# Kernel tuning notes

Measured on AMD Instinct MI355X. Metric: run time of the kernel, lower is better.

Reference implementation:

```python
import jax, jax.numpy as jnp
import numpy as np

N0, N1, N2 = 512, 2048, 8192   # targets, hop1, hop2 node counts
K = 33                          # nneighbor + self loop
IN, HID, OUT, NH = 256, 128, 128, 8
NEG = -9.0e15
ALPHA = 0.2                     # LeakyReLU negative slope


def setup_inputs() -> dict:
    key = jax.random.key(0)
    ks = jax.random.split(key, 8)
    feats = jax.random.normal(ks[0], (N2, IN), jnp.float32)
    # xavier-ish scaled params (gain 1.414)
    W1 = jax.random.normal(ks[1], (NH, IN, HID), jnp.float32) * 0.072
    a1 = jax.random.normal(ks[2], (NH, 2 * HID), jnp.float32) * 0.105
    W2 = jax.random.normal(ks[3], (HID * NH, OUT), jnp.float32) * 0.042
    a2 = jax.random.normal(ks[4], (2 * OUT,), jnp.float32) * 0.105
    # layer1 edges: each of N1 targets gets K distinct neighbors in [0, N2)
    tgt1 = jnp.repeat(jnp.arange(N1, dtype=jnp.int32), K)
    dst1 = ((jnp.arange(N1)[:, None] * 97 + jnp.arange(K)[None, :] * 131) % N2).astype(jnp.int32).reshape(-1)
    src1 = jax.random.randint(ks[5], (N1 * K,), 0, N2, jnp.int32)
    # layer2 edges: each of N0 targets gets K distinct neighbors in [0, N1)
    tgt2 = jnp.repeat(jnp.arange(N0, dtype=jnp.int32), K)
    dst2 = ((jnp.arange(N0)[:, None] * 53 + jnp.arange(K)[None, :] * 61) % N1).astype(jnp.int32).reshape(-1)
    src2 = jax.random.randint(ks[6], (N0 * K,), 0, N1, jnp.int32)
    return dict(feats=feats, W1=W1, a1=a1, W2=W2, a2=a2,
                src1=src1, dst1=dst1, tgt1=tgt1, src2=src2, dst2=dst2, tgt2=tgt2)


def gat_layer(x, W, a, src, dst, tgt, t_len):
    # x: [n, in], W: [in, d], a: [2d]
    h = x @ W                                   # [n, d]
    d = h.shape[1]
    # concat([h[src], h[dst]]) @ a  ==  h[src]@a[:d] + h[dst]@a[d:]
    e = h[src] @ a[:d] + h[dst] @ a[d:]         # [E]
    e = jnp.where(e > 0, e, ALPHA * e)          # LeakyReLU
    att = jnp.full((t_len, h.shape[0]), NEG, h.dtype).at[tgt, dst].set(e)
    att = jax.nn.softmax(att, axis=1)           # dense row softmax (masked entries ~0)
    return jax.nn.elu(att @ h)                  # [t_len, d]


def reference(feats, W1, a1, W2, a2, src1, dst1, tgt1, src2, dst2, tgt2):
    # layer 1: nhead independent GAT heads over hop2 features
    heads = jax.vmap(lambda W, a: gat_layer(feats, W, a, src1, dst1, tgt1, N1))(W1, a1)  # [NH, N1, HID]
    x = jnp.transpose(heads, (1, 0, 2)).reshape(N1, NH * HID)  # torch.cat(dim=1)
    # layer 2: single GAT layer producing [N0, OUT]
    return gat_layer(x, W2, a2, src2, dst2, tgt2, N0)
```

## Files before the change

### kernel.cpp

```cpp
#include <hip/hip_runtime.h>
#include <math.h>

#define ALPHA 0.2f

constexpr int CN0 = 512, CN1 = 2048, CN2 = 8192, CK = 33;
constexpr int CIN = 256, CHID = 128, CNH = 8;

using u16    = unsigned short;
using f32x4  = __attribute__((ext_vector_type(4))) float;
using bf16x8 = __attribute__((ext_vector_type(8))) short;

__device__ __forceinline__ u16 f2bf(float f) {
    unsigned u = __float_as_uint(f);
    u += 0x7fff + ((u >> 16) & 1);
    return (u16)(u >> 16);
}
__device__ __forceinline__ float bf2f(u16 h) {
    return __uint_as_float(((unsigned)h) << 16);
}

#define GLD16(g, l)                                                        \
    __builtin_amdgcn_global_load_lds(                                      \
        (const __attribute__((address_space(1))) void*)(g),                \
        (__attribute__((address_space(3))) void*)(l), 16, 0, 0)

__global__ __launch_bounds__(256) void prep2_k(const float* __restrict__ W1,
                                               u16* __restrict__ w1t,
                                               const float* __restrict__ W2,
                                               u16* __restrict__ w2t,
                                               const float* __restrict__ a1,
                                               float* __restrict__ pvec) {
    __shared__ float t[32][33];
    int b = blockIdx.x;
    if (b >= 384) {
        const int i = b - 384;
        const int h = i >> 1, half = i & 1;
        const int j = threadIdx.x;
        const float* wrow = W1 + (size_t)h * CIN * CHID + (size_t)j * CHID;
        const float* ah   = a1 + h * 2 * CHID + half * CHID;
        float d = 0.f;
#pragma unroll 8
        for (int c = 0; c < CHID; ++c) d = fmaf(wrow[c], ah[c], d);
        pvec[(h * 2 + half) * CIN + j] = d;
        return;
    }
    const float* ip;
    u16* op;
    int R, C, r0, c0;
    if (b < 256) {
        const int h = b >> 5, w = b & 31;
        ip = W1 + (size_t)h * CIN * CHID;
        op = w1t + (size_t)h * CIN * CHID;
        R = CIN; C = CHID; r0 = (w >> 2) * 32; c0 = (w & 3) * 32;
    } else {
        b -= 256;
        ip = W2; op = w2t;
        R = CNH * CHID; C = CHID; r0 = (b >> 2) * 32; c0 = (b & 3) * 32;
    }
    const int tx = threadIdx.x & 31, ty = threadIdx.x >> 5;
#pragma unroll
    for (int i = 0; i < 4; ++i)
        t[ty + 8 * i][tx] = ip[(size_t)(r0 + ty + 8 * i) * C + c0 + tx];
    __syncthreads();
#pragma unroll
    for (int i = 0; i < 4; ++i)
        op[(size_t)(c0 + ty + 8 * i) * R + r0 + tx] = f2bf(t[tx][ty + 8 * i]);
}

__global__ __launch_bounds__(256) void fsc_k(const float* __restrict__ feats,
                                             u16* __restrict__ fb,
                                             const float* __restrict__ pvec,
                                             float* __restrict__ s1,
                                             float* __restrict__ s2) {
    const int node = (blockIdx.x * 256 + threadIdx.x) >> 6;
    const int lane = threadIdx.x & 63;
    const float4 v = *reinterpret_cast<const float4*>(feats + (size_t)node * CIN + lane * 4);
    *reinterpret_cast<ushort4*>(fb + (size_t)node * CIN + lane * 4) =
        make_ushort4(f2bf(v.x), f2bf(v.y), f2bf(v.z), f2bf(v.w));
#pragma unroll
    for (int h = 0; h < CNH; ++h) {
        const float4 p1 = *reinterpret_cast<const float4*>(pvec + (h * 2 + 0) * CIN + lane * 4);
        const float4 p2 = *reinterpret_cast<const float4*>(pvec + (h * 2 + 1) * CIN + lane * 4);
        float d1 = v.x * p1.x + v.y * p1.y + v.z * p1.z + v.w * p1.w;
        float d2 = v.x * p2.x + v.y * p2.y + v.z * p2.z + v.w * p2.w;
#pragma unroll
        for (int m = 1; m < 64; m <<= 1) {
            d1 += __shfl_xor(d1, m);
            d2 += __shfl_xor(d2, m);
        }
        if (lane == 0) {
            s1[h * CN2 + node] = d1;
            s2[h * CN2 + node] = d2;
        }
    }
}

__global__ __launch_bounds__(128) void agg1g_k(const float* __restrict__ s1,
                                               const float* __restrict__ s2,
                                               const int* __restrict__ src,
                                               const int* __restrict__ dst,
                                               const u16* __restrict__ fb,
                                               u16* __restrict__ gb) {
    __shared__ float wgt[CNH][CK];
    __shared__ int dsts[CK];

    const int t    = blockIdx.x;
    const int tid  = threadIdx.x;
    const int wv   = tid >> 6;
    const int lane = tid & 63;

    int sv = 0, dv = 0;
    if (lane < CK) {
        sv = src[t * CK + lane];
        dv = dst[t * CK + lane];
        if (tid < CK) dsts[tid] = dv;
    }
#pragma unroll
    for (int hh = 0; hh < 4; ++hh) {
        const int head = wv * 4 + hh;
        float e = -3.0e38f;
        if (lane < CK) {
            const float ee = s1[head * CN2 + sv] + s2[head * CN2 + dv];
            e = (ee > 0.f) ? ee : ALPHA * ee;
        }
        float m = e;
#pragma unroll
        for (int mm = 1; mm < 64; mm <<= 1) m = fmaxf(m, __shfl_xor(m, mm));
        const float p = (lane < CK) ? __expf(e - m) : 0.f;
        float s = p;
#pragma unroll
        for (int mm = 1; mm < 64; mm <<= 1) s += __shfl_xor(s, mm);
        if (lane < CK) wgt[head][lane] = p / s;
    }
    __syncthreads();

    const int c2 = tid * 2;
    float acc[CNH][2];
#pragma unroll
    for (int h = 0; h < CNH; ++h) { acc[h][0] = 0.f; acc[h][1] = 0.f; }
#pragma unroll 4
    for (int k = 0; k < CK; ++k) {
        const unsigned w2 = *reinterpret_cast<const unsigned*>(
            fb + (size_t)dsts[k] * CIN + c2);
        const float f0 = bf2f((u16)(w2 & 0xffff));
        const float f1 = bf2f((u16)(w2 >> 16));
#pragma unroll
        for (int h = 0; h < CNH; ++h) {
            const float wk = wgt[h][k];
            acc[h][0] = fmaf(wk, f0, acc[h][0]);
            acc[h][1] = fmaf(wk, f1, acc[h][1]);
        }
    }
#pragma unroll
    for (int h = 0; h < CNH; ++h) {
        const unsigned o = ((unsigned)f2bf(acc[h][1]) << 16) | f2bf(acc[h][0]);
        *reinterpret_cast<unsigned*>(gb + ((size_t)h * CN1 + t) * CIN + c2) = o;
    }
}

__global__ __launch_bounds__(256) void fusedproj_k(const u16* __restrict__ gb,
                                                   const u16* __restrict__ w1t,
                                                   const u16* __restrict__ w2t,
                                                   float* __restrict__ part) {
    __shared__ __attribute__((aligned(16))) char smem[24576];

    const int tid  = threadIdx.x;
    const int lane = tid & 63;
    const int wave = tid >> 6;
    const int trow0 = blockIdx.x * 64;
    const int h     = blockIdx.y;
    const int wr = (wave >> 1) * 32;
    const int wc = (wave & 1) * 64;

    const u16* A  = gb  + (size_t)h * CN1 * CIN;
    const u16* Bt = w1t + (size_t)h * CHID * CIN;

    f32x4 acc[2][4];
#pragma unroll
    for (int m = 0; m < 2; ++m)
#pragma unroll
        for (int n = 0; n < 4; ++n) acc[m][n] = (f32x4){0.f, 0.f, 0.f, 0.f};

    const int r0c = tid >> 2;
    const int cs0 = tid & 3;
    const int c0  = (cs0 - (r0c >> 1)) & 3;
    const int r1c = r0c + 64;

    const u16* ga0 = A + (size_t)(trow0 + r0c) * CIN + c0 * 8;
    const u16* gb0 = Bt + (size_t)r0c * CIN + c0 * 8;
    const u16* gb1 = Bt + (size_t)r1c * CIN + c0 * 8;

    auto STAGE = [&](int s) {
        const int k0 = s * 32;
        char* base = smem + (s & 1) * 12288;
        u16* as = (u16*)base + wave * 512;
        u16* bs = (u16*)(base + 4096) + wave * 512;
        GLD16(ga0 + k0, as);
        GLD16(gb0 + k0, bs);
        GLD16(gb1 + k0, bs + 2048);
    };

    STAGE(0);
    __syncthreads();

    for (int s = 0; s < 8; ++s) {
        if (s + 1 < 8) STAGE(s + 1);

        const u16* Acur = (const u16*)(smem + (s & 1) * 12288);
        const u16* Bcur = Acur + 2048;

        bf16x8 af[2], bfr[4];
#pragma unroll
        for (int m = 0; m < 2; ++m) {
            const int rt = wr + m * 16 + (lane & 15);
            const int cs = ((lane >> 4) + (rt >> 1)) & 3;
            af[m] = *reinterpret_cast<const bf16x8*>(Acur + rt * 32 + cs * 8);
        }
#pragma unroll
        for (int n = 0; n < 4; ++n) {
            const int rt2 = wc + n * 16 + (lane & 15);
            const int cs2 = ((lane >> 4) + (rt2 >> 1)) & 3;
            bfr[n] = *reinterpret_cast<const bf16x8*>(Bcur + rt2 * 32 + cs2 * 8);
        }
#pragma unroll
        for (int m = 0; m < 2; ++m)
#pragma unroll
            for (int n = 0; n < 4; ++n)
                acc[m][n] = __builtin_amdgcn_mfma_f32_16x16x32_bf16(
                    af[m], bfr[n], acc[m][n], 0, 0, 0);

        __syncthreads();
    }

    u16* Xs = (u16*)smem;
#pragma unroll
    for (int m = 0; m < 2; ++m) {
        const int rr = wr + m * 16 + (lane >> 4) * 4;
#pragma unroll
        for (int n = 0; n < 4; ++n) {
            const int cc = wc + n * 16 + (lane & 15);
#pragma unroll
            for (int q = 0; q < 4; ++q) {
                float v = acc[m][n][q];
                v = (v > 0.f) ? v : __expf(v) - 1.f;
                const int r = rr + q;
                Xs[r * 128 + ((((cc >> 3) ^ (r & 7)) << 3) | (cc & 7))] = f2bf(v);
            }
        }
    }
    __syncthreads();

    f32x4 acc2[2][4];
#pragma unroll
    for (int m = 0; m < 2; ++m)
#pragma unroll
        for (int n = 0; n < 4; ++n) acc2[m][n] = (f32x4){0.f, 0.f, 0.f, 0.f};

#pragma unroll
    for (int ks = 0; ks < 4; ++ks) {
        bf16x8 a2f[2], b2f[4];
#pragma unroll
        for (int m = 0; m < 2; ++m) {
            const int rt = wr + m * 16 + (lane & 15);
            const int k0 = ks * 32 + (lane >> 4) * 8;
            a2f[m] = *reinterpret_cast<const bf16x8*>(
                Xs + rt * 128 + (((k0 >> 3) ^ (rt & 7)) << 3));
        }
#pragma unroll
        for (int n = 0; n < 4; ++n) {
            const int rb = wc + n * 16 + (lane & 15);
            b2f[n] = *reinterpret_cast<const bf16x8*>(
                w2t + (size_t)rb * (CNH * CHID) + h * CHID + ks * 32 + (lane >> 4) * 8);
        }
#pragma unroll
        for (int m = 0; m < 2; ++m)
#pragma unroll
            for (int n = 0; n < 4; ++n)
                acc2[m][n] = __builtin_amdgcn_mfma_f32_16x16x32_bf16(
                    a2f[m], b2f[n], acc2[m][n], 0, 0, 0);
    }

#pragma unroll
    for (int m = 0; m < 2; ++m) {
        const int rr = trow0 + wr + m * 16 + (lane >> 4) * 4;
#pragma unroll
        for (int n = 0; n < 4; ++n) {
            const int cc = wc + n * 16 + (lane & 15);
#pragma unroll
            for (int q = 0; q < 4; ++q)
                part[((size_t)h * CN1 + rr + q) * CHID + cc] = acc2[m][n][q];
        }
    }
}

__global__ __launch_bounds__(256) void scores2_k(const float* __restrict__ part,
                                                 const float* __restrict__ a,
                                                 float* __restrict__ h2,
                                                 float* __restrict__ s1,
                                                 float* __restrict__ s2) {
    const int wid  = (blockIdx.x * 256 + threadIdx.x) >> 6;
    const int lane = threadIdx.x & 63;
    const int j = lane * 2;
    float x0 = 0.f, x1 = 0.f;
#pragma unroll
    for (int sp = 0; sp < 8; ++sp) {
        const float2 v = *reinterpret_cast<const float2*>(
            part + (size_t)sp * CN1 * CHID + (size_t)wid * CHID + j);
        x0 += v.x; x1 += v.y;
    }
    *reinterpret_cast<float2*>(h2 + (size_t)wid * CHID + j) = make_float2(x0, x1);
    float d1 = x0 * a[j] + x1 * a[j + 1];
    float d2 = x0 * a[CHID + j] + x1 * a[CHID + j + 1];
#pragma unroll
    for (int m = 1; m < 64; m <<= 1) {
        d1 += __shfl_xor(d1, m);
        d2 += __shfl_xor(d2, m);
    }
    if (lane == 0) { s1[wid] = d1; s2[wid] = d2; }
}

__global__ __launch_bounds__(256) void agg2_k(const float* __restrict__ s1,
                                              const float* __restrict__ s2,
                                              const int* __restrict__ src,
                                              const int* __restrict__ dst,
                                              const float* __restrict__ h2,
                                              float* __restrict__ out) {
    const int t    = (blockIdx.x * 256 + threadIdx.x) >> 6;
    const int lane = threadIdx.x & 63;

    float e = -3.0e38f;
    int dv = 0;
    if (lane < CK) {
        const int sv = src[t * CK + lane];
        dv = dst[t * CK + lane];
        const float ee = s1[sv] + s2[dv];
        e = (ee > 0.f) ? ee : ALPHA * ee;
    }
    float m = e;
#pragma unroll
    for (int mm = 1; mm < 64; mm <<= 1) m = fmaxf(m, __shfl_xor(m, mm));
    float p = (lane < CK) ? __expf(e - m) : 0.f;
    float ssum = p;
#pragma unroll
    for (int mm = 1; mm < 64; mm <<= 1) ssum += __shfl_xor(ssum, mm);
    const float invs = 1.f / ssum;

    float a0 = 0.f, a1 = 0.f;
#pragma unroll
    for (int k = 0; k < CK; ++k) {
        const float w = __shfl(p, k) * invs;
        const int d = __shfl(dv, k);
        const float2 hv = *reinterpret_cast<const float2*>(h2 + (size_t)d * CHID + lane * 2);
        a0 = fmaf(w, hv.x, a0);
        a1 = fmaf(w, hv.y, a1);
    }
    a0 = (a0 > 0.f) ? a0 : __expf(a0) - 1.f;
    a1 = (a1 > 0.f) ? a1 : __expf(a1) - 1.f;
    *reinterpret_cast<float2*>(out + (size_t)t * CHID + lane * 2) = make_float2(a0, a1);
}

extern "C" void kernel_launch(void* const* d_in, const int* in_sizes, int n_in,
                              void* d_out, int out_size, void* d_ws, size_t ws_size,
                              hipStream_t stream) {
    const float* feats = (const float*)d_in[0];
    const float* W1    = (const float*)d_in[1];
    const float* a1    = (const float*)d_in[2];
    const float* W2    = (const float*)d_in[3];
    const float* a2    = (const float*)d_in[4];
    const int*   src1  = (const int*)d_in[5];
    const int*   dst1  = (const int*)d_in[6];
    const int*   src2  = (const int*)d_in[8];
    const int*   dst2  = (const int*)d_in[9];
    float* out = (float*)d_out;

    char* w = (char*)d_ws;
    u16*   fb   = (u16*)w;                 w += (size_t)CN2 * CIN * 2;
    u16*   w1t  = (u16*)w;                 w += (size_t)CNH * CIN * CHID * 2;
    u16*   w2t  = (u16*)w;                 w += (size_t)CNH * CHID * CHID * 2;
    float* pvec = (float*)w;               w += (size_t)CNH * 2 * CIN * 4;
    float* s1   = (float*)w;               w += (size_t)CNH * CN2 * 4;
    float* s2   = (float*)w;               w += (size_t)CNH * CN2 * 4;
    u16*   gb   = (u16*)w;                 w += (size_t)CNH * CN1 * CIN * 2;
    float* part = (float*)w;               w += (size_t)8 * CN1 * CHID * 4;
    float* h2   = (float*)w;               w += (size_t)CN1 * CHID * 4;
    float* s21  = (float*)w;               w += (size_t)CN1 * 4;
    float* s22  = (float*)w;               w += (size_t)CN1 * 4;

    prep2_k<<<dim3(256 + 128 + 16), 256, 0, stream>>>(W1, w1t, W2, w2t, a1, pvec);

    fsc_k<<<dim3(CN2 / 4), 256, 0, stream>>>(feats, fb, pvec, s1, s2);

    agg1g_k<<<dim3(CN1), 128, 0, stream>>>(s1, s2, src1, dst1, fb, gb);

    fusedproj_k<<<dim3(CN1 / 64, CNH), 256, 0, stream>>>(gb, w1t, w2t, part);

    scores2_k<<<dim3(CN1 / 4), 256, 0, stream>>>(part, a2, h2, s21, s22);

    agg2_k<<<dim3(CN0 / 4), 256, 0, stream>>>(s21, s22, src2, dst2, h2, out);
}
```

Baseline: 52.81 us.

## Fuse head loop into projection kernel, accumulate layer-2 in registers, fold scores

The projection kernel now loops over all 8 heads inside one block of 32 rows and accumulates the second-layer product in registers. This removes the per-head partial buffer and the separate reduction/score kernel, which now runs as an epilogue computing h2 and the attention score dot products. The weight transpose is also merged into the feature-conversion kernel, and pvec gets its own small kernel. In exchange the projection grid drops from 256 blocks to 64, which lowers parallelism and lengthens the serial K loop per block.

```diff
diff --git a/kernel.cpp b/kernel.cpp
--- a/kernel.cpp
+++ b/kernel.cpp
@@ -24,26 +24,55 @@
         (const __attribute__((address_space(1))) void*)(g),                \
         (__attribute__((address_space(3))) void*)(l), 16, 0, 0)
 
-__global__ __launch_bounds__(256) void prep2_k(const float* __restrict__ W1,
-                                               u16* __restrict__ w1t,
-                                               const float* __restrict__ W2,
-                                               u16* __restrict__ w2t,
-                                               const float* __restrict__ a1,
-                                               float* __restrict__ pvec) {
+__global__ __launch_bounds__(256) void pvec_k(const float* __restrict__ W1,
+                                              const float* __restrict__ a1,
+                                              float* __restrict__ pvec) {
+    const int h = blockIdx.x >> 1, half = blockIdx.x & 1;
+    const int j = threadIdx.x;
+    const float* wrow = W1 + (size_t)h * CIN * CHID + (size_t)j * CHID;
+    const float* ah   = a1 + h * 2 * CHID + half * CHID;
+    float d = 0.f;
+#pragma unroll 8
+    for (int c = 0; c < CHID; ++c) d = fmaf(wrow[c], ah[c], d);
+    pvec[(h * 2 + half) * CIN + j] = d;
+}
+
+__global__ __launch_bounds__(256) void fsc_k(const float* __restrict__ feats,
+                                             u16* __restrict__ fb,
+                                             const float* __restrict__ pvec,
+                                             float* __restrict__ s1,
+                                             float* __restrict__ s2,
+                                             const float* __restrict__ W1,
+                                             u16* __restrict__ w1t,
+                                             const float* __restrict__ W2,
+                                             u16* __restrict__ w2t) {
     __shared__ float t[32][33];
     int b = blockIdx.x;
-    if (b >= 384) {
-        const int i = b - 384;
-        const int h = i >> 1, half = i & 1;
-        const int j = threadIdx.x;
-        const float* wrow = W1 + (size_t)h * CIN * CHID + (size_t)j * CHID;
-        const float* ah   = a1 + h * 2 * CHID + half * CHID;
-        float d = 0.f;
-#pragma unroll 8
-        for (int c = 0; c < CHID; ++c) d = fmaf(wrow[c], ah[c], d);
-        pvec[(h * 2 + half) * CIN + j] = d;
+    if (b < 2048) {
+        const int node = (b * 256 + threadIdx.x) >> 6;
+        const int lane = threadIdx.x & 63;
+        const float4 v = *reinterpret_cast<const float4*>(feats + (size_t)node * CIN + lane * 4);
+        *reinterpret_cast<ushort4*>(fb + (size_t)node * CIN + lane * 4) =
+            make_ushort4(f2bf(v.x), f2bf(v.y), f2bf(v.z), f2bf(v.w));
+#pragma unroll
+        for (int h = 0; h < CNH; ++h) {
+            const float4 p1 = *reinterpret_cast<const float4*>(pvec + (h * 2 + 0) * CIN + lane * 4);
+            const float4 p2 = *reinterpret_cast<const float4*>(pvec + (h * 2 + 1) * CIN + lane * 4);
+            float d1 = v.x * p1.x + v.y * p1.y + v.z * p1.z + v.w * p1.w;
+            float d2 = v.x * p2.x + v.y * p2.y + v.z * p2.z + v.w * p2.w;
+#pragma unroll
+            for (int m = 1; m < 64; m <<= 1) {
+                d1 += __shfl_xor(d1, m);
+                d2 += __shfl_xor(d2, m);
+            }
+            if (lane == 0) {
+                s1[h * CN2 + node] = d1;
+                s2[h * CN2 + node] = d2;
+            }
+        }
         return;
     }
+    b -= 2048;
     const float* ip;
     u16* op;
     int R, C, r0, c0;
@@ -67,34 +96,6 @@
         op[(size_t)(c0 + ty + 8 * i) * R + r0 + tx] = f2bf(t[tx][ty + 8 * i]);
 }
 
-__global__ __launch_bounds__(256) void fsc_k(const float* __restrict__ feats,
-                                             u16* __restrict__ fb,
-                                             const float* __restrict__ pvec,
-                                             float* __restrict__ s1,
-                                             float* __restrict__ s2) {
-    const int node = (blockIdx.x * 256 + threadIdx.x) >> 6;
-    const int lane = threadIdx.x & 63;
-    const float4 v = *reinterpret_cast<const float4*>(feats + (size_t)node * CIN + lane * 4);
-    *reinterpret_cast<ushort4*>(fb + (size_t)node * CIN + lane * 4) =
-        make_ushort4(f2bf(v.x), f2bf(v.y), f2bf(v.z), f2bf(v.w));
-#pragma unroll
-    for (int h = 0; h < CNH; ++h) {
-        const float4 p1 = *reinterpret_cast<const float4*>(pvec + (h * 2 + 0) * CIN + lane * 4);
-        const float4 p2 = *reinterpret_cast<const float4*>(pvec + (h * 2 + 1) * CIN + lane * 4);
-        float d1 = v.x * p1.x + v.y * p1.y + v.z * p1.z + v.w * p1.w;
-        float d2 = v.x * p2.x + v.y * p2.y + v.z * p2.z + v.w * p2.w;
-#pragma unroll
-        for (int m = 1; m < 64; m <<= 1) {
-            d1 += __shfl_xor(d1, m);
-            d2 += __shfl_xor(d2, m);
-        }
-        if (lane == 0) {
-            s1[h * CN2 + node] = d1;
-            s2[h * CN2 + node] = d2;
-        }
-    }
-}
-
 __global__ __launch_bounds__(128) void agg1g_k(const float* __restrict__ s1,
                                                const float* __restrict__ s2,
                                                const int* __restrict__ src,
@@ -140,10 +141,10 @@
     for (int h = 0; h < CNH; ++h) { acc[h][0] = 0.f; acc[h][1] = 0.f; }
 #pragma unroll 4
     for (int k = 0; k < CK; ++k) {
-        const unsigned w2 = *reinterpret_cast<const unsigned*>(
+        const unsigned w2v = *reinterpret_cast<const unsigned*>(
             fb + (size_t)dsts[k] * CIN + c2);
-        const float f0 = bf2f((u16)(w2 & 0xffff));
-        const float f1 = bf2f((u16)(w2 >> 16));
+        const float f0 = bf2f((u16)(w2v & 0xffff));
+        const float f1 = bf2f((u16)(w2v >> 16));
 #pragma unroll
         for (int h = 0; h < CNH; ++h) {
             const float wk = wgt[h][k];
@@ -158,165 +159,167 @@
     }
 }
 
-__global__ __launch_bounds__(256) void fusedproj_k(const u16* __restrict__ gb,
-                                                   const u16* __restrict__ w1t,
-                                                   const u16* __restrict__ w2t,
-                                                   float* __restrict__ part) {
-    __shared__ __attribute__((aligned(16))) char smem[24576];
+__global__ __launch_bounds__(256) void fusedproj2_k(const u16* __restrict__ gb,
+                                                    const u16* __restrict__ w1t,
+                                                    const u16* __restrict__ w2t,
+                                                    const float* __restrict__ a2,
+                                                    float* __restrict__ h2,
+                                                    float* __restrict__ s21,
+                                                    float* __restrict__ s22) {
+    __shared__ __attribute__((aligned(16))) char smem[20480];
+    __shared__ __attribute__((aligned(16))) u16 Xs[32 * 128];
+    __shared__ float sred1[2][32];
+    __shared__ float sred2[2][32];
 
     const int tid  = threadIdx.x;
     const int lane = tid & 63;
-    const int wave = tid >> 6;
-    const int trow0 = blockIdx.x * 64;
-    const int h     = blockIdx.y;
-    const int wr = (wave >> 1) * 32;
-    const int wc = (wave & 1) * 64;
-
-    const u16* A  = gb  + (size_t)h * CN1 * CIN;
-    const u16* Bt = w1t + (size_t)h * CHID * CIN;
-
-    f32x4 acc[2][4];
-#pragma unroll
-    for (int m = 0; m < 2; ++m)
-#pragma unroll
-        for (int n = 0; n < 4; ++n) acc[m][n] = (f32x4){0.f, 0.f, 0.f, 0.f};
+    const int wv   = tid >> 6;
+    const int trow0 = blockIdx.x * 32;
+    const int wr = (wv >> 1) * 16;
+    const int wc = (wv & 1) * 64;
 
     const int r0c = tid >> 2;
-    const int cs0 = tid & 3;
-    const int c0  = (cs0 - (r0c >> 1)) & 3;
+    const int c0  = ((tid & 3) - (r0c >> 1)) & 3;
     const int r1c = r0c + 64;
-
-    const u16* ga0 = A + (size_t)(trow0 + r0c) * CIN + c0 * 8;
-    const u16* gb0 = Bt + (size_t)r0c * CIN + c0 * 8;
-    const u16* gb1 = Bt + (size_t)r1c * CIN + c0 * 8;
-
-    auto STAGE = [&](int s) {
-        const int k0 = s * 32;
-        char* base = smem + (s & 1) * 12288;
-        u16* as = (u16*)base + wave * 512;
-        u16* bs = (u16*)(base + 4096) + wave * 512;
-        GLD16(ga0 + k0, as);
-        GLD16(gb0 + k0, bs);
-        GLD16(gb1 + k0, bs + 2048);
+    const int rA = (tid & 127) >> 2;
+    const int cA = ((tid & 3) - (rA >> 1)) & 3;
+
+    f32x4 acc2[4];
+#pragma unroll
+    for (int n = 0; n < 4; ++n) acc2[n] = (f32x4){0.f, 0.f, 0.f, 0.f};
+
+    auto STAGE = [&](int g) {
+        const int h = g >> 3, k0 = (g & 7) * 32;
+        char* base = smem + (g & 1) * 10240;
+        const u16* A  = gb  + (size_t)h * CN1 * CIN;
+        const u16* Bt = w1t + (size_t)h * CHID * CIN;
+        if (wv < 2) {
+            u16* as = (u16*)base + wv * 512;
+            GLD16(A + (size_t)(trow0 + rA) * CIN + k0 + cA * 8, as);
+        }
+        u16* bs = (u16*)(base + 2048) + wv * 512;
+        GLD16(Bt + (size_t)r0c * CIN + k0 + c0 * 8, bs);
+        GLD16(Bt + (size_t)r1c * CIN + k0 + c0 * 8, bs + 2048);
     };
 
     STAGE(0);
     __syncthreads();
 
-    for (int s = 0; s < 8; ++s) {
-        if (s + 1 < 8) STAGE(s + 1);
-
-        const u16* Acur = (const u16*)(smem + (s & 1) * 12288);
-        const u16* Bcur = Acur + 2048;
-
-        bf16x8 af[2], bfr[4];
-#pragma unroll
-        for (int m = 0; m < 2; ++m) {
-            const int rt = wr + m * 16 + (lane & 15);
-            const int cs = ((lane >> 4) + (rt >> 1)) & 3;
-            af[m] = *reinterpret_cast<const bf16x8*>(Acur + rt * 32 + cs * 8);
-        }
+    for (int h = 0; h < CNH; ++h) {
+        f32x4 acc[4];
+#pragma unroll
+        for (int n = 0; n < 4; ++n) acc[n] = (f32x4){0.f, 0.f, 0.f, 0.f};
+
+        for (int s = 0; s < 8; ++s) {
+            const int g = h * 8 + s;
+            if (g + 1 < 64) STAGE(g + 1);
+
+            const u16* Acur = (const u16*)(smem + (g & 1) * 10240);
+            const u16* Bcur = Acur + 1024;
+
+            bf16x8 af, bfr[4];
+            {
+                const int rt = wr + (lane & 15);
+                const int cs = ((lane >> 4) + (rt >> 1)) & 3;
+                af = *reinterpret_cast<const bf16x8*>(Acur + rt * 32 + cs * 8);
+            }
+#pragma unroll
+            for (int n = 0; n < 4; ++n) {
+                const int rt2 = wc + n * 16 + (lane & 15);
+                const int cs2 = ((lane >> 4) + (rt2 >> 1)) & 3;
+                bfr[n] = *reinterpret_cast<const bf16x8*>(Bcur + rt2 * 32 + cs2 * 8);
+            }
+#pragma unroll
+            for (int n = 0; n < 4; ++n)
+                acc[n] = __builtin_amdgcn_mfma_f32_16x16x32_bf16(af, bfr[n], acc[n], 0, 0, 0);
+
+            __syncthreads();
+        }
+
+        {
+            const int rr = wr + (lane >> 4) * 4;
+#pragma unroll
+            for (int n = 0; n < 4; ++n) {
+                const int cc = wc + n * 16 + (lane & 15);
+#pragma unroll
+                for (int q = 0; q < 4; ++q) {
+                    float v = acc[n][q];
+                    v = (v > 0.f) ? v : __expf(v) - 1.f;
+                    const int r = rr + q;
+                    Xs[r * 128 + ((((cc >> 3) ^ (r & 7)) << 3) | (cc & 7))] = f2bf(v);
+                }
+            }
+        }
+        __syncthreads();
+
+#pragma unroll
+        for (int ks = 0; ks < 4; ++ks) {
+            bf16x8 a2f, b2f[4];
+            {
+                const int rt = wr + (lane & 15);
+                const int k0 = ks * 32 + (lane >> 4) * 8;
+                a2f = *reinterpret_cast<const bf16x8*>(
+                    Xs + rt * 128 + (((k0 >> 3) ^ (rt & 7)) << 3));
+            }
+#pragma unroll
+            for (int n = 0; n < 4; ++n) {
+                const int rb = wc + n * 16 + (lane & 15);
+                b2f[n] = *reinterpret_cast<const bf16x8*>(
+                    w2t + (size_t)rb * (CNH * CHID) + h * CHID + ks * 32 + (lane >> 4) * 8);
+            }
+#pragma unroll
+            for (int n = 0; n < 4; ++n)
+                acc2[n] = __builtin_amdgcn_mfma_f32_16x16x32_bf16(a2f, b2f[n], acc2[n], 0, 0, 0);
+        }
+        __syncthreads();
+    }
+
+    const int rrow = wr + (lane >> 4) * 4;
+#pragma unroll
+    for (int n = 0; n < 4; ++n) {
+        const int cc = wc + n * 16 + (lane & 15);
+#pragma unroll
+        for (int q = 0; q < 4; ++q)
+            h2[(size_t)(trow0 + rrow + q) * CHID + cc] = acc2[n][q];
+    }
+
+    float av1[4], av2[4];
+#pragma unroll
+    for (int n = 0; n < 4; ++n) {
+        const int c = wc + n * 16 + (lane & 15);
+        av1[n] = a2[c];
+        av2[n] = a2[CHID + c];
+    }
+    float p1[4], p2[4];
+#pragma unroll
+    for (int q = 0; q < 4; ++q) {
+        float t1 = 0.f, t2 = 0.f;
 #pragma unroll
         for (int n = 0; n < 4; ++n) {
-            const int rt2 = wc + n * 16 + (lane & 15);
-            const int cs2 = ((lane >> 4) + (rt2 >> 1)) & 3;
-            bfr[n] = *reinterpret_cast<const bf16x8*>(Bcur + rt2 * 32 + cs2 * 8);
-        }
-#pragma unroll
-        for (int m = 0; m < 2; ++m)
-#pragma unroll
-            for (int n = 0; n < 4; ++n)
-                acc[m][n] = __builtin_amdgcn_mfma_f32_16x16x32_bf16(
-                    af[m], bfr[n], acc[m][n], 0, 0, 0);
-
-        __syncthreads();
-    }
-
-    u16* Xs = (u16*)smem;
-#pragma unroll
-    for (int m = 0; m < 2; ++m) {
-        const int rr = wr + m * 16 + (lane >> 4) * 4;
-#pragma unroll
-        for (int n = 0; n < 4; ++n) {
-            const int cc = wc + n * 16 + (lane & 15);
-#pragma unroll
-            for (int q = 0; q < 4; ++q) {
-                float v = acc[m][n][q];
-                v = (v > 0.f) ? v : __expf(v) - 1.f;
-                const int r = rr + q;
-                Xs[r * 128 + ((((cc >> 3) ^ (r & 7)) << 3) | (cc & 7))] = f2bf(v);
-            }
+            t1 = fmaf(acc2[n][q], av1[n], t1);
+            t2 = fmaf(acc2[n][q], av2[n], t2);
+        }
+#pragma unroll
+        for (int mk = 1; mk < 16; mk <<= 1) {
+            t1 += __shfl_xor(t1, mk);
+            t2 += __shfl_xor(t2, mk);
+        }
+        p1[q] = t1;
+        p2[q] = t2;
+    }
+    if ((lane & 15) == 0) {
+        const int g = lane >> 4;
+#pragma unroll
+        for (int q = 0; q < 4; ++q) {
+            sred1[wv & 1][wr + g * 4 + q] = p1[q];
+            sred2[wv & 1][wr + g * 4 + q] = p2[q];
         }
     }
     __syncthreads();
-
-    f32x4 acc2[2][4];
-#pragma unroll
-    for (int m = 0; m < 2; ++m)
-#pragma unroll
-        for (int n = 0; n < 4; ++n) acc2[m][n] = (f32x4){0.f, 0.f, 0.f, 0.f};
-
-#pragma unroll
-    for (int ks = 0; ks < 4; ++ks) {
-        bf16x8 a2f[2], b2f[4];
-#pragma unroll
-        for (int m = 0; m < 2; ++m) {
-            const int rt = wr + m * 16 + (lane & 15);
-            const int k0 = ks * 32 + (lane >> 4) * 8;
-            a2f[m] = *reinterpret_cast<const bf16x8*>(
-                Xs + rt * 128 + (((k0 >> 3) ^ (rt & 7)) << 3));
-        }
-#pragma unroll
-        for (int n = 0; n < 4; ++n) {
-            const int rb = wc + n * 16 + (lane & 15);
-            b2f[n] = *reinterpret_cast<const bf16x8*>(
-                w2t + (size_t)rb * (CNH * CHID) + h * CHID + ks * 32 + (lane >> 4) * 8);
-        }
-#pragma unroll
-        for (int m = 0; m < 2; ++m)
-#pragma unroll
-            for (int n = 0; n < 4; ++n)
-                acc2[m][n] = __builtin_amdgcn_mfma_f32_16x16x32_bf16(
-                    a2f[m], b2f[n], acc2[m][n], 0, 0, 0);
-    }
-
-#pragma unroll
-    for (int m = 0; m < 2; ++m) {
-        const int rr = trow0 + wr + m * 16 + (lane >> 4) * 4;
-#pragma unroll
-        for (int n = 0; n < 4; ++n) {
-            const int cc = wc + n * 16 + (lane & 15);
-#pragma unroll
-            for (int q = 0; q < 4; ++q)
-                part[((size_t)h * CN1 + rr + q) * CHID + cc] = acc2[m][n][q];
-        }
-    }
-}
-
-__global__ __launch_bounds__(256) void scores2_k(const float* __restrict__ part,
-                                                 const float* __restrict__ a,
-                                                 float* __restrict__ h2,
-                                                 float* __restrict__ s1,
-                                                 float* __restrict__ s2) {
-    const int wid  = (blockIdx.x * 256 + threadIdx.x) >> 6;
-    const int lane = threadIdx.x & 63;
-    const int j = lane * 2;
-    float x0 = 0.f, x1 = 0.f;
-#pragma unroll
-    for (int sp = 0; sp < 8; ++sp) {
-        const float2 v = *reinterpret_cast<const float2*>(
-            part + (size_t)sp * CN1 * CHID + (size_t)wid * CHID + j);
-        x0 += v.x; x1 += v.y;
-    }
-    *reinterpret_cast<float2*>(h2 + (size_t)wid * CHID + j) = make_float2(x0, x1);
-    float d1 = x0 * a[j] + x1 * a[j + 1];
-    float d2 = x0 * a[CHID + j] + x1 * a[CHID + j + 1];
-#pragma unroll
-    for (int m = 1; m < 64; m <<= 1) {
-        d1 += __shfl_xor(d1, m);
-        d2 += __shfl_xor(d2, m);
-    }
-    if (lane == 0) { s1[wid] = d1; s2[wid] = d2; }
+    if (tid < 32) {
+        s21[trow0 + tid] = sred1[0][tid] + sred1[1][tid];
+        s22[trow0 + tid] = sred2[0][tid] + sred2[1][tid];
+    }
 }
 
 __global__ __launch_bounds__(256) void agg2_k(const float* __restrict__ s1,
@@ -381,20 +384,18 @@
     float* s1   = (float*)w;               w += (size_t)CNH * CN2 * 4;
     float* s2   = (float*)w;               w += (size_t)CNH * CN2 * 4;
     u16*   gb   = (u16*)w;                 w += (size_t)CNH * CN1 * CIN * 2;
-    float* part = (float*)w;               w += (size_t)8 * CN1 * CHID * 4;
     float* h2   = (float*)w;               w += (size_t)CN1 * CHID * 4;
     float* s21  = (float*)w;               w += (size_t)CN1 * 4;
     float* s22  = (float*)w;               w += (size_t)CN1 * 4;
 
-    prep2_k<<<dim3(256 + 128 + 16), 256, 0, stream>>>(W1, w1t, W2, w2t, a1, pvec);
-
-    fsc_k<<<dim3(CN2 / 4), 256, 0, stream>>>(feats, fb, pvec, s1, s2);
+    pvec_k<<<dim3(16), 256, 0, stream>>>(W1, a1, pvec);
+
+    fsc_k<<<dim3(2048 + 256 + 128), 256, 0, stream>>>(
+        feats, fb, pvec, s1, s2, W1, w1t, W2, w2t);
 
     agg1g_k<<<dim3(CN1), 128, 0, stream>>>(s1, s2, src1, dst1, fb, gb);
 
-    fusedproj_k<<<dim3(CN1 / 64, CNH), 256, 0, stream>>>(gb, w1t, w2t, part);
-
-    scores2_k<<<dim3(CN1 / 4), 256, 0, stream>>>(part, a2, h2, s21, s22);
+    fusedproj2_k<<<dim3(CN1 / 32), 256, 0, stream>>>(gb, w1t, w2t, a2, h2, s21, s22);
 
     agg2_k<<<dim3(CN0 / 4), 256, 0, stream>>>(s21, s22, src2, dst2, h2, out);
 }
```

Result: slower. 83.31 us (+57.8%).

## Fuse scores2 into projection via last-block atomic counter; merge prep into fsc

Applied to the files above, without the earlier changes.

The standalone scores2 kernel is removed. Each projection block now bumps a per-row-tile atomic counter, and the last of the 8 head blocks for a tile reduces the partial sums and computes the layer-2 scores. The weight transpose/convert work moves into the fsc kernel's grid, and a tiny new pvec kernel computes pvec and zeroes the counters. Together this drops one kernel launch and overlaps the weight prep with feature conversion. In exchange the reduction is serialized onto one block per tile and relies on threadfence/atomic correctness.

```diff
diff --git a/kernel.cpp b/kernel.cpp
--- a/kernel.cpp
+++ b/kernel.cpp
@@ -24,26 +24,60 @@
         (const __attribute__((address_space(1))) void*)(g),                \
         (__attribute__((address_space(3))) void*)(l), 16, 0, 0)
 
-__global__ __launch_bounds__(256) void prep2_k(const float* __restrict__ W1,
-                                               u16* __restrict__ w1t,
-                                               const float* __restrict__ W2,
-                                               u16* __restrict__ w2t,
-                                               const float* __restrict__ a1,
-                                               float* __restrict__ pvec) {
+__global__ __launch_bounds__(256) void pvec_k(const float* __restrict__ W1,
+                                              const float* __restrict__ a1,
+                                              float* __restrict__ pvec,
+                                              int* __restrict__ cnt) {
+    if (blockIdx.x == 16) {
+        if (threadIdx.x < 32) cnt[threadIdx.x] = 0;
+        return;
+    }
+    const int h = blockIdx.x >> 1, half = blockIdx.x & 1;
+    const int j = threadIdx.x;
+    const float* wrow = W1 + (size_t)h * CIN * CHID + (size_t)j * CHID;
+    const float* ah   = a1 + h * 2 * CHID + half * CHID;
+    float d = 0.f;
+#pragma unroll 8
+    for (int c = 0; c < CHID; ++c) d = fmaf(wrow[c], ah[c], d);
+    pvec[(h * 2 + half) * CIN + j] = d;
+}
+
+__global__ __launch_bounds__(256) void fsc_k(const float* __restrict__ feats,
+                                             u16* __restrict__ fb,
+                                             const float* __restrict__ pvec,
+                                             float* __restrict__ s1,
+                                             float* __restrict__ s2,
+                                             const float* __restrict__ W1,
+                                             u16* __restrict__ w1t,
+                                             const float* __restrict__ W2,
+                                             u16* __restrict__ w2t) {
     __shared__ float t[32][33];
     int b = blockIdx.x;
-    if (b >= 384) {
-        const int i = b - 384;
-        const int h = i >> 1, half = i & 1;
-        const int j = threadIdx.x;
-        const float* wrow = W1 + (size_t)h * CIN * CHID + (size_t)j * CHID;
-        const float* ah   = a1 + h * 2 * CHID + half * CHID;
-        float d = 0.f;
-#pragma unroll 8
-        for (int c = 0; c < CHID; ++c) d = fmaf(wrow[c], ah[c], d);
-        pvec[(h * 2 + half) * CIN + j] = d;
+    if (b < 2048) {
+        const int node = (b * 256 + threadIdx.x) >> 6;
+        const int lane = threadIdx.x & 63;
+        const float4 v = *reinterpret_cast<const float4*>(feats + (size_t)node * CIN + lane * 4);
+        *reinterpret_cast<ushort4*>(fb + (size_t)node * CIN + lane * 4) =
+            make_ushort4(f2bf(v.x), f2bf(v.y), f2bf(v.z), f2bf(v.w));
+#pragma unroll
+        for (int h = 0; h < CNH; ++h) {
+            const float4 p1 = *reinterpret_cast<const float4*>(pvec + (h * 2 + 0) * CIN + lane * 4);
+            const float4 p2 = *reinterpret_cast<const float4*>(pvec + (h * 2 + 1) * CIN + lane * 4);
+            float d1 = v.x * p1.x + v.y * p1.y + v.z * p1.z + v.w * p1.w;
+            float d2 = v.x * p2.x + v.y * p2.y + v.z * p2.z + v.w * p2.w;
+#pragma unroll
+            for (int m = 1; m < 64; m <<= 1) {
+                d1 += __shfl_xor(d1, m);
+                d2 += __shfl_xor(d2, m);
+            }
+            if (lane == 0) {
+                s1[h * CN2 + node] = d1;
+                s2[h * CN2 + node] = d2;
+            }
+        }
         return;
     }
+    b -= 2048;
     const float* ip;
     u16* op;
     int R, C, r0, c0;
@@ -67,34 +101,6 @@
         op[(size_t)(c0 + ty + 8 * i) * R + r0 + tx] = f2bf(t[tx][ty + 8 * i]);
 }
 
-__global__ __launch_bounds__(256) void fsc_k(const float* __restrict__ feats,
-                                             u16* __restrict__ fb,
-                                             const float* __restrict__ pvec,
-                                             float* __restrict__ s1,
-                                             float* __restrict__ s2) {
-    const int node = (blockIdx.x * 256 + threadIdx.x) >> 6;
-    const int lane = threadIdx.x & 63;
-    const float4 v = *reinterpret_cast<const float4*>(feats + (size_t)node * CIN + lane * 4);
-    *reinterpret_cast<ushort4*>(fb + (size_t)node * CIN + lane * 4) =
-        make_ushort4(f2bf(v.x), f2bf(v.y), f2bf(v.z), f2bf(v.w));
-#pragma unroll
-    for (int h = 0; h < CNH; ++h) {
-        const float4 p1 = *reinterpret_cast<const float4*>(pvec + (h * 2 + 0) * CIN + lane * 4);
-        const float4 p2 = *reinterpret_cast<const float4*>(pvec + (h * 2 + 1) * CIN + lane * 4);
-        float d1 = v.x * p1.x + v.y * p1.y + v.z * p1.z + v.w * p1.w;
-        float d2 = v.x * p2.x + v.y * p2.y + v.z * p2.z + v.w * p2.w;
-#pragma unroll
-        for (int m = 1; m < 64; m <<= 1) {
-            d1 += __shfl_xor(d1, m);
-            d2 += __shfl_xor(d2, m);
-        }
-        if (lane == 0) {
-            s1[h * CN2 + node] = d1;
-            s2[h * CN2 + node] = d2;
-        }
-    }
-}
-
 __global__ __launch_bounds__(128) void agg1g_k(const float* __restrict__ s1,
                                                const float* __restrict__ s2,
                                                const int* __restrict__ src,
@@ -140,10 +146,10 @@
     for (int h = 0; h < CNH; ++h) { acc[h][0] = 0.f; acc[h][1] = 0.f; }
 #pragma unroll 4
     for (int k = 0; k < CK; ++k) {
-        const unsigned w2 = *reinterpret_cast<const unsigned*>(
+        const unsigned w2v = *reinterpret_cast<const unsigned*>(
             fb + (size_t)dsts[k] * CIN + c2);
-        const float f0 = bf2f((u16)(w2 & 0xffff));
-        const float f1 = bf2f((u16)(w2 >> 16));
+        const float f0 = bf2f((u16)(w2v & 0xffff));
+        const float f1 = bf2f((u16)(w2v >> 16));
 #pragma unroll
         for (int h = 0; h < CNH; ++h) {
             const float wk = wgt[h][k];
@@ -161,13 +167,20 @@
 __global__ __launch_bounds__(256) void fusedproj_k(const u16* __restrict__ gb,
                                                    const u16* __restrict__ w1t,
                                                    const u16* __restrict__ w2t,
-                                                   float* __restrict__ part) {
+                                                   const float* __restrict__ a2,
+                                                   float* __restrict__ part,
+                                                   float* __restrict__ h2,
+                                                   float* __restrict__ s21,
+                                                   float* __restrict__ s22,
+                                                   int* __restrict__ cnt) {
     __shared__ __attribute__((aligned(16))) char smem[24576];
+    __shared__ int flag;
 
     const int tid  = threadIdx.x;
     const int lane = tid & 63;
     const int wave = tid >> 6;
-    const int trow0 = blockIdx.x * 64;
+    const int tile  = blockIdx.x;
+    const int trow0 = tile * 64;
     const int h     = blockIdx.y;
     const int wr = (wave >> 1) * 32;
     const int wc = (wave & 1) * 64;
@@ -291,32 +304,34 @@
                 part[((size_t)h * CN1 + rr + q) * CHID + cc] = acc2[m][n][q];
         }
     }
-}
-
-__global__ __launch_bounds__(256) void scores2_k(const float* __restrict__ part,
-                                                 const float* __restrict__ a,
-                                                 float* __restrict__ h2,
-                                                 float* __restrict__ s1,
-                                                 float* __restrict__ s2) {
-    const int wid  = (blockIdx.x * 256 + threadIdx.x) >> 6;
-    const int lane = threadIdx.x & 63;
-    const int j = lane * 2;
-    float x0 = 0.f, x1 = 0.f;
-#pragma unroll
-    for (int sp = 0; sp < 8; ++sp) {
-        const float2 v = *reinterpret_cast<const float2*>(
-            part + (size_t)sp * CN1 * CHID + (size_t)wid * CHID + j);
-        x0 += v.x; x1 += v.y;
-    }
-    *reinterpret_cast<float2*>(h2 + (size_t)wid * CHID + j) = make_float2(x0, x1);
-    float d1 = x0 * a[j] + x1 * a[j + 1];
-    float d2 = x0 * a[CHID + j] + x1 * a[CHID + j + 1];
-#pragma unroll
-    for (int m = 1; m < 64; m <<= 1) {
-        d1 += __shfl_xor(d1, m);
-        d2 += __shfl_xor(d2, m);
-    }
-    if (lane == 0) { s1[wid] = d1; s2[wid] = d2; }
+
+    __threadfence();
+    __syncthreads();
+    if (tid == 0) flag = atomicAdd(&cnt[tile], 1);
+    __syncthreads();
+    if (flag != CNH - 1) return;
+    __threadfence();
+
+    for (int it = 0; it < 16; ++it) {
+        const int node = trow0 + wave * 16 + it;
+        const int j = lane * 2;
+        float x0 = 0.f, x1 = 0.f;
+#pragma unroll
+        for (int sp = 0; sp < 8; ++sp) {
+            const float2 v = *reinterpret_cast<const float2*>(
+                part + ((size_t)sp * CN1 + node) * CHID + j);
+            x0 += v.x; x1 += v.y;
+        }
+        *reinterpret_cast<float2*>(h2 + (size_t)node * CHID + j) = make_float2(x0, x1);
+        float d1 = x0 * a2[j] + x1 * a2[j + 1];
+        float d2 = x0 * a2[CHID + j] + x1 * a2[CHID + j + 1];
+#pragma unroll
+        for (int m = 1; m < 64; m <<= 1) {
+            d1 += __shfl_xor(d1, m);
+            d2 += __shfl_xor(d2, m);
+        }
+        if (lane == 0) { s21[node] = d1; s22[node] = d2; }
+    }
 }
 
 __global__ __launch_bounds__(256) void agg2_k(const float* __restrict__ s1,
@@ -385,16 +400,17 @@
     float* h2   = (float*)w;               w += (size_t)CN1 * CHID * 4;
     float* s21  = (float*)w;               w += (size_t)CN1 * 4;
     float* s22  = (float*)w;               w += (size_t)CN1 * 4;
-
-    prep2_k<<<dim3(256 + 128 + 16), 256, 0, stream>>>(W1, w1t, W2, w2t, a1, pvec);
-
-    fsc_k<<<dim3(CN2 / 4), 256, 0, stream>>>(feats, fb, pvec, s1, s2);
+    int*   cnt  = (int*)w;                 w += 32 * 4;
+
+    pvec_k<<<dim3(17), 256, 0, stream>>>(W1, a1, pvec, cnt);
+
+    fsc_k<<<dim3(2048 + 256 + 128), 256, 0, stream>>>(
+        feats, fb, pvec, s1, s2, W1, w1t, W2, w2t);
 
     agg1g_k<<<dim3(CN1), 128, 0, stream>>>(s1, s2, src1, dst1, fb, gb);
 
-    fusedproj_k<<<dim3(CN1 / 64, CNH), 256, 0, stream>>>(gb, w1t, w2t, part);
-
-    scores2_k<<<dim3(CN1 / 4), 256, 0, stream>>>(part, a2, h2, s21, s22);
+    fusedproj_k<<<dim3(CN1 / 64, CNH), 256, 0, stream>>>(
+        gb, w1t, w2t, a2, part, h2, s21, s22, cnt);
 
     agg2_k<<<dim3(CN0 / 4), 256, 0, stream>>>(s21, s22, src2, dst2, h2, out);
 }
```

Measured after the change: 94.76 us. 79.5% more time.

## Fuse pipeline into four kernels by computing attention scores on the fly

Applied to the files above, without the earlier changes.

Folds the feature bf16 conversion into the weight-prep kernel and drops the separate per-node score kernel. Layer-1 scores are now recomputed inside the aggregation kernel from gathered bf16 features for each edge's src and dst. The head-sum, layer-2 scores and layer-2 aggregation are merged into a single per-target kernel that reduces the partial projections on demand. This removes two kernel launches and the intermediate score/h2 buffers, at the cost of redundant score and partial-sum recomputation across targets and lower-precision (bf16) features in the layer-1 scores.

```diff
diff --git a/kernel.cpp b/kernel.cpp
--- a/kernel.cpp
+++ b/kernel.cpp
@@ -24,16 +24,25 @@
         (const __attribute__((address_space(1))) void*)(g),                \
         (__attribute__((address_space(3))) void*)(l), 16, 0, 0)
 
-__global__ __launch_bounds__(256) void prep2_k(const float* __restrict__ W1,
-                                               u16* __restrict__ w1t,
-                                               const float* __restrict__ W2,
-                                               u16* __restrict__ w2t,
-                                               const float* __restrict__ a1,
-                                               float* __restrict__ pvec) {
+__global__ __launch_bounds__(256) void prep_k(const float* __restrict__ feats,
+                                              u16* __restrict__ fb,
+                                              const float* __restrict__ W1,
+                                              u16* __restrict__ w1t,
+                                              const float* __restrict__ W2,
+                                              u16* __restrict__ w2t,
+                                              const float* __restrict__ a1,
+                                              float* __restrict__ pvec) {
     __shared__ float t[32][33];
     int b = blockIdx.x;
-    if (b >= 384) {
-        const int i = b - 384;
+    if (b < 2048) {
+        const int i = (b * 256 + threadIdx.x) * 4;
+        const float4 v = *reinterpret_cast<const float4*>(feats + i);
+        *reinterpret_cast<ushort4*>(fb + i) =
+            make_ushort4(f2bf(v.x), f2bf(v.y), f2bf(v.z), f2bf(v.w));
+        return;
+    }
+    if (b >= 2432) {
+        const int i = b - 2432;
         const int h = i >> 1, half = i & 1;
         const int j = threadIdx.x;
         const float* wrow = W1 + (size_t)h * CIN * CHID + (size_t)j * CHID;
@@ -44,6 +53,7 @@
         pvec[(h * 2 + half) * CIN + j] = d;
         return;
     }
+    b -= 2048;
     const float* ip;
     u16* op;
     int R, C, r0, c0;
@@ -67,60 +77,67 @@
         op[(size_t)(c0 + ty + 8 * i) * R + r0 + tx] = f2bf(t[tx][ty + 8 * i]);
 }
 
-__global__ __launch_bounds__(256) void fsc_k(const float* __restrict__ feats,
-                                             u16* __restrict__ fb,
-                                             const float* __restrict__ pvec,
-                                             float* __restrict__ s1,
-                                             float* __restrict__ s2) {
-    const int node = (blockIdx.x * 256 + threadIdx.x) >> 6;
-    const int lane = threadIdx.x & 63;
-    const float4 v = *reinterpret_cast<const float4*>(feats + (size_t)node * CIN + lane * 4);
-    *reinterpret_cast<ushort4*>(fb + (size_t)node * CIN + lane * 4) =
-        make_ushort4(f2bf(v.x), f2bf(v.y), f2bf(v.z), f2bf(v.w));
-#pragma unroll
-    for (int h = 0; h < CNH; ++h) {
-        const float4 p1 = *reinterpret_cast<const float4*>(pvec + (h * 2 + 0) * CIN + lane * 4);
-        const float4 p2 = *reinterpret_cast<const float4*>(pvec + (h * 2 + 1) * CIN + lane * 4);
-        float d1 = v.x * p1.x + v.y * p1.y + v.z * p1.z + v.w * p1.w;
-        float d2 = v.x * p2.x + v.y * p2.y + v.z * p2.z + v.w * p2.w;
-#pragma unroll
-        for (int m = 1; m < 64; m <<= 1) {
-            d1 += __shfl_xor(d1, m);
-            d2 += __shfl_xor(d2, m);
-        }
-        if (lane == 0) {
-            s1[h * CN2 + node] = d1;
-            s2[h * CN2 + node] = d2;
-        }
-    }
-}
-
-__global__ __launch_bounds__(128) void agg1g_k(const float* __restrict__ s1,
-                                               const float* __restrict__ s2,
-                                               const int* __restrict__ src,
-                                               const int* __restrict__ dst,
-                                               const u16* __restrict__ fb,
-                                               u16* __restrict__ gb) {
+__global__ __launch_bounds__(128) void agg1g2_k(const float* __restrict__ pvec,
+                                                const int* __restrict__ src,
+                                                const int* __restrict__ dst,
+                                                const u16* __restrict__ fb,
+                                                u16* __restrict__ gb) {
+    __shared__ float sc[2][CK][CNH];
     __shared__ float wgt[CNH][CK];
-    __shared__ int dsts[CK];
+    __shared__ int nds[2][CK];
 
     const int t    = blockIdx.x;
     const int tid  = threadIdx.x;
     const int wv   = tid >> 6;
     const int lane = tid & 63;
 
-    int sv = 0, dv = 0;
-    if (lane < CK) {
-        sv = src[t * CK + lane];
-        dv = dst[t * CK + lane];
-        if (tid < CK) dsts[tid] = dv;
-    }
+    if (tid < CK) {
+        nds[0][tid] = src[t * CK + tid];
+        nds[1][tid] = dst[t * CK + tid];
+    }
+    __syncthreads();
+
+    for (int k = wv; k < CK; k += 2) {
+#pragma unroll
+        for (int type = 0; type < 2; ++type) {
+            const int n = nds[type][k];
+            const ushort4 fv = *reinterpret_cast<const ushort4*>(
+                fb + (size_t)n * CIN + lane * 4);
+            const float f0 = bf2f(fv.x), f1 = bf2f(fv.y);
+            const float f2 = bf2f(fv.z), f3 = bf2f(fv.w);
+            float p0, p1, p2, p3, p4, p5, p6, p7;
+#define DOT(H, P)                                                              \
+            {                                                                  \
+                const float4 pv = *reinterpret_cast<const float4*>(            \
+                    pvec + (H * 2 + type) * CIN + lane * 4);                   \
+                P = f0 * pv.x + f1 * pv.y + f2 * pv.z + f3 * pv.w;             \
+            }
+            DOT(0, p0) DOT(1, p1) DOT(2, p2) DOT(3, p3)
+            DOT(4, p4) DOT(5, p5) DOT(6, p6) DOT(7, p7)
+#undef DOT
+#pragma unroll
+            for (int m = 1; m < 64; m <<= 1) {
+                p0 += __shfl_xor(p0, m); p1 += __shfl_xor(p1, m);
+                p2 += __shfl_xor(p2, m); p3 += __shfl_xor(p3, m);
+                p4 += __shfl_xor(p4, m); p5 += __shfl_xor(p5, m);
+                p6 += __shfl_xor(p6, m); p7 += __shfl_xor(p7, m);
+            }
+            if (lane == 0) {
+                sc[type][k][0] = p0; sc[type][k][1] = p1;
+                sc[type][k][2] = p2; sc[type][k][3] = p3;
+                sc[type][k][4] = p4; sc[type][k][5] = p5;
+                sc[type][k][6] = p6; sc[type][k][7] = p7;
+            }
+        }
+    }
+    __syncthreads();
+
 #pragma unroll
     for (int hh = 0; hh < 4; ++hh) {
         const int head = wv * 4 + hh;
         float e = -3.0e38f;
         if (lane < CK) {
-            const float ee = s1[head * CN2 + sv] + s2[head * CN2 + dv];
+            const float ee = sc[0][lane][head] + sc[1][lane][head];
             e = (ee > 0.f) ? ee : ALPHA * ee;
         }
         float m = e;
@@ -140,10 +157,10 @@
     for (int h = 0; h < CNH; ++h) { acc[h][0] = 0.f; acc[h][1] = 0.f; }
 #pragma unroll 4
     for (int k = 0; k < CK; ++k) {
-        const unsigned w2 = *reinterpret_cast<const unsigned*>(
-            fb + (size_t)dsts[k] * CIN + c2);
-        const float f0 = bf2f((u16)(w2 & 0xffff));
-        const float f1 = bf2f((u16)(w2 >> 16));
+        const unsigned w2v = *reinterpret_cast<const unsigned*>(
+            fb + (size_t)nds[1][k] * CIN + c2);
+        const float f0 = bf2f((u16)(w2v & 0xffff));
+        const float f1 = bf2f((u16)(w2v >> 16));
 #pragma unroll
         for (int h = 0; h < CNH; ++h) {
             const float wk = wgt[h][k];
@@ -293,70 +310,85 @@
     }
 }
 
-__global__ __launch_bounds__(256) void scores2_k(const float* __restrict__ part,
-                                                 const float* __restrict__ a,
-                                                 float* __restrict__ h2,
-                                                 float* __restrict__ s1,
-                                                 float* __restrict__ s2) {
-    const int wid  = (blockIdx.x * 256 + threadIdx.x) >> 6;
-    const int lane = threadIdx.x & 63;
-    const int j = lane * 2;
-    float x0 = 0.f, x1 = 0.f;
-#pragma unroll
-    for (int sp = 0; sp < 8; ++sp) {
-        const float2 v = *reinterpret_cast<const float2*>(
-            part + (size_t)sp * CN1 * CHID + (size_t)wid * CHID + j);
-        x0 += v.x; x1 += v.y;
-    }
-    *reinterpret_cast<float2*>(h2 + (size_t)wid * CHID + j) = make_float2(x0, x1);
-    float d1 = x0 * a[j] + x1 * a[j + 1];
-    float d2 = x0 * a[CHID + j] + x1 * a[CHID + j + 1];
-#pragma unroll
-    for (int m = 1; m < 64; m <<= 1) {
-        d1 += __shfl_xor(d1, m);
-        d2 += __shfl_xor(d2, m);
-    }
-    if (lane == 0) { s1[wid] = d1; s2[wid] = d2; }
-}
-
-__global__ __launch_bounds__(256) void agg2_k(const float* __restrict__ s1,
-                                              const float* __restrict__ s2,
-                                              const int* __restrict__ src,
-                                              const int* __restrict__ dst,
-                                              const float* __restrict__ h2,
-                                              float* __restrict__ out) {
-    const int t    = (blockIdx.x * 256 + threadIdx.x) >> 6;
-    const int lane = threadIdx.x & 63;
-
-    float e = -3.0e38f;
-    int dv = 0;
-    if (lane < CK) {
-        const int sv = src[t * CK + lane];
-        dv = dst[t * CK + lane];
-        const float ee = s1[sv] + s2[dv];
-        e = (ee > 0.f) ? ee : ALPHA * ee;
-    }
-    float m = e;
-#pragma unroll
-    for (int mm = 1; mm < 64; mm <<= 1) m = fmaxf(m, __shfl_xor(m, mm));
-    float p = (lane < CK) ? __expf(e - m) : 0.f;
-    float ssum = p;
-#pragma unroll
-    for (int mm = 1; mm < 64; mm <<= 1) ssum += __shfl_xor(ssum, mm);
-    const float invs = 1.f / ssum;
-
-    float a0 = 0.f, a1 = 0.f;
-#pragma unroll
+__global__ __launch_bounds__(128) void final_k(const float* __restrict__ part,
+                                               const float* __restrict__ a2,
+                                               const int* __restrict__ src,
+                                               const int* __restrict__ dst,
+                                               float* __restrict__ out) {
+    __shared__ float h2row[CK][CHID];
+    __shared__ float e1[CK], e2[CK], wgt[CK];
+    __shared__ int nds[2][CK];
+
+    const int t    = blockIdx.x;
+    const int tid  = threadIdx.x;
+    const int wv   = tid >> 6;
+    const int lane = tid & 63;
+
+    if (tid < CK) {
+        nds[0][tid] = src[t * CK + tid];
+        nds[1][tid] = dst[t * CK + tid];
+    }
+    __syncthreads();
+
     for (int k = 0; k < CK; ++k) {
-        const float w = __shfl(p, k) * invs;
-        const int d = __shfl(dv, k);
-        const float2 hv = *reinterpret_cast<const float2*>(h2 + (size_t)d * CHID + lane * 2);
-        a0 = fmaf(w, hv.x, a0);
-        a1 = fmaf(w, hv.y, a1);
-    }
-    a0 = (a0 > 0.f) ? a0 : __expf(a0) - 1.f;
-    a1 = (a1 > 0.f) ? a1 : __expf(a1) - 1.f;
-    *reinterpret_cast<float2*>(out + (size_t)t * CHID + lane * 2) = make_float2(a0, a1);
+        const int dv = nds[1][k];
+        float x = 0.f;
+#pragma unroll
+        for (int sp = 0; sp < 8; ++sp)
+            x += part[((size_t)sp * CN1 + dv) * CHID + tid];
+        h2row[k][tid] = x;
+    }
+    __syncthreads();
+
+    if (wv == 0) {
+        for (int k = 0; k < CK; ++k) {
+            const int sv = nds[0][k];
+            const int j = lane * 2;
+            float x0 = 0.f, x1 = 0.f;
+#pragma unroll
+            for (int sp = 0; sp < 8; ++sp) {
+                const float2 v = *reinterpret_cast<const float2*>(
+                    part + ((size_t)sp * CN1 + sv) * CHID + j);
+                x0 += v.x; x1 += v.y;
+            }
+            float d = x0 * a2[j] + x1 * a2[j + 1];
+#pragma unroll
+            for (int m = 1; m < 64; m <<= 1) d += __shfl_xor(d, m);
+            if (lane == 0) e1[k] = d;
+        }
+    } else {
+        for (int k = 0; k < CK; ++k) {
+            const int j = lane * 2;
+            float d = h2row[k][j] * a2[CHID + j] + h2row[k][j + 1] * a2[CHID + j + 1];
+#pragma unroll
+            for (int m = 1; m < 64; m <<= 1) d += __shfl_xor(d, m);
+            if (lane == 0) e2[k] = d;
+        }
+    }
+    __syncthreads();
+
+    if (wv == 0) {
+        float e = -3.0e38f;
+        if (lane < CK) {
+            const float ee = e1[lane] + e2[lane];
+            e = (ee > 0.f) ? ee : ALPHA * ee;
+        }
+        float m = e;
+#pragma unroll
+        for (int mm = 1; mm < 64; mm <<= 1) m = fmaxf(m, __shfl_xor(m, mm));
+        const float p = (lane < CK) ? __expf(e - m) : 0.f;
+        float s = p;
+#pragma unroll
+        for (int mm = 1; mm < 64; mm <<= 1) s += __shfl_xor(s, mm);
+        if (lane < CK) wgt[lane] = p / s;
+    }
+    __syncthreads();
+
+    float acc = 0.f;
+#pragma unroll
+    for (int k = 0; k < CK; ++k)
+        acc = fmaf(wgt[k], h2row[k][tid], acc);
+    out[(size_t)t * CHID + tid] = (acc > 0.f) ? acc : __expf(acc) - 1.f;
 }
 
 extern "C" void kernel_launch(void* const* d_in, const int* in_sizes, int n_in,
@@ -378,23 +410,15 @@
     u16*   w1t  = (u16*)w;                 w += (size_t)CNH * CIN * CHID * 2;
     u16*   w2t  = (u16*)w;                 w += (size_t)CNH * CHID * CHID * 2;
     float* pvec = (float*)w;               w += (size_t)CNH * 2 * CIN * 4;
-    float* s1   = (float*)w;               w += (size_t)CNH * CN2 * 4;
-    float* s2   = (float*)w;               w += (size_t)CNH * CN2 * 4;
     u16*   gb   = (u16*)w;                 w += (size_t)CNH * CN1 * CIN * 2;
     float* part = (float*)w;               w += (size_t)8 * CN1 * CHID * 4;
-    float* h2   = (float*)w;               w += (size_t)CN1 * CHID * 4;
-    float* s21  = (float*)w;               w += (size_t)CN1 * 4;
-    float* s22  = (float*)w;               w += (size_t)CN1 * 4;
-
-    prep2_k<<<dim3(256 + 128 + 16), 256, 0, stream>>>(W1, w1t, W2, w2t, a1, pvec);
-
-    fsc_k<<<dim3(CN2 / 4), 256, 0, stream>>>(feats, fb, pvec, s1, s2);
-
-    agg1g_k<<<dim3(CN1), 128, 0, stream>>>(s1, s2, src1, dst1, fb, gb);
+
+    prep_k<<<dim3(2048 + 256 + 128 + 16), 256, 0, stream>>>(
+        feats, fb, W1, w1t, W2, w2t, a1, pvec);
+
+    agg1g2_k<<<dim3(CN1), 128, 0, stream>>>(pvec, src1, dst1, fb, gb);
 
     fusedproj_k<<<dim3(CN1 / 64, CNH), 256, 0, stream>>>(gb, w1t, w2t, part);
 
-    scores2_k<<<dim3(CN1 / 4), 256, 0, stream>>>(part, a2, h2, s21, s22);
-
-    agg2_k<<<dim3(CN0 / 4), 256, 0, stream>>>(s21, s22, src2, dst2, h2, out);
-}
+    final_k<<<dim3(CN0), 128, 0, stream>>>(part, a2, src2, dst2, out);
+}
```

Result: slower. 172.0 us (+225.6%).
